# Kernel optimization log

Measured on AMD Instinct MI355X. Metric: run time of the kernel, lower is better.

The kernel has to match this reference:

```python
import jax, jax.numpy as jnp
import numpy as np

ALPHA = 0.2          # LeakyReLU negative slope
ORTHO_LAMBDA = 0.01  # orthogonal regularization weight


def setup_inputs() -> dict:
    key = jax.random.key(0)
    ks = jax.random.split(key, 9)
    N, IN, OUT, NR, H = 50000, 128, 128, 64, 4
    E1, E2 = 200000, 50000
    return {
        "input": jax.random.normal(ks[0], (N, IN), jnp.float32),
        "edge": jax.random.randint(ks[1], (2, E1), 0, N),
        "edge_embed": jax.random.normal(ks[2], (E1, NR), jnp.float32),
        "edge_list_nhop": jax.random.randint(ks[3], (2, E2), 0, N),
        "edge_embed_nhop": jax.random.normal(ks[4], (E2, NR), jnp.float32),
        "proj": jax.random.normal(ks[5], (H, IN, IN), jnp.float32) / np.sqrt(IN).astype(np.float32),
        "W": jax.random.normal(ks[6], (H, OUT, 2 * IN + NR), jnp.float32) * 0.08,
        "a": jax.random.normal(ks[7], (H, 1, OUT), jnp.float32) * 0.1,
        "head_weights": jnp.ones((H,), jnp.float32),
    }


def reference(input, edge, edge_embed, edge_list_nhop, edge_embed_nhop, proj, W, a, head_weights):
    N, IN = input.shape
    H, OUT, _ = W.shape
    e = jnp.concatenate([edge, edge_list_nhop], axis=1)              # [2, E]
    emb = jnp.concatenate([edge_embed, edge_embed_nhop], axis=0)     # [E, NR]
    src, tgt = e[0], e[1]

    # per-head orthogonal projections: head_input[h] = input @ proj[h].T -> [H, N, IN]
    hin = jnp.einsum('ni,hoi->hno', input, proj)

    # edge_m = W @ concat(h_src, h_tgt, rel) without materializing the concat
    W_src, W_tgt, W_rel = W[:, :, :IN], W[:, :, IN:2 * IN], W[:, :, 2 * IN:]
    edge_m = (jnp.einsum('hei,hoi->heo', hin[:, src, :], W_src)
              + jnp.einsum('hei,hoi->heo', hin[:, tgt, :], W_tgt)
              + jnp.einsum('er,hor->heo', emb, W_rel))               # [H, E, OUT]

    scores = jnp.einsum('heo,ho->he', edge_m, a[:, 0, :])            # [H, E]
    powers = -jnp.where(scores > 0, scores, ALPHA * scores)         # -leakyrelu
    edge_e = jnp.exp(powers)                                         # [H, E]

    seg = lambda v: jax.ops.segment_sum(v, src, num_segments=N)
    e_rowsum = jnp.clip(jax.vmap(seg)(edge_e), 1e-12, None)          # [H, N]

    edge_w = edge_e[:, :, None] * edge_m                             # [H, E, OUT]
    head_out = jax.vmap(seg)(edge_w)                                 # [H, N, OUT]

    w = jax.nn.softmax(head_weights)
    out = jnp.einsum('h,hnd->nd', w, head_out)                       # [N, OUT]
    # faithful to torch: divides by the LAST head's e_rowsum (loop leakage)
    out = out / e_rowsum[-1][:, None]

    pp = jnp.einsum('hij,hkj->hik', proj, proj)                      # proj @ proj.T
    eye = jnp.eye(proj.shape[1], dtype=proj.dtype)
    orth_reg = ORTHO_LAMBDA * jnp.sum(jnp.sqrt(jnp.sum((pp - eye) ** 2, axis=(1, 2))))

    return jax.nn.elu(out), orth_reg
```

## Files before the change

### kernel.cpp

```cpp
#include <hip/hip_runtime.h>
#include <math.h>


#define NHEAD 4

typedef unsigned short u16;
typedef __attribute__((ext_vector_type(4))) unsigned short u16x4;
typedef __attribute__((ext_vector_type(8))) unsigned short u16x8;
typedef __attribute__((ext_vector_type(8))) short bf16x8;
typedef __attribute__((ext_vector_type(4))) float f32x4;

__device__ __forceinline__ float bf2f(u16 v) {
    union { unsigned u; float f; } x; x.u = ((unsigned)v) << 16; return x.f;
}
__device__ __forceinline__ u16 f2bf(float f) {
    union { float f; unsigned u; } x; x.f = f;
    const unsigned r = x.u + 0x7FFFu + ((x.u >> 16) & 1u);
    return (u16)(r >> 16);
}

__global__ __launch_bounds__(256) void k1_prep(
    const float* __restrict__ proj, const float* __restrict__ W,
    const float* __restrict__ a, const float* __restrict__ hw,
    u16* __restrict__ M_bf,
    float* __restrict__ asrc, float* __restrict__ atgt, float* __restrict__ arel,
    u16* __restrict__ WcatT_bf, float* __restrict__ wsoft,
    float* __restrict__ orth_part)
{
    __shared__ float projS[128*132];
    __shared__ float WS[32*132];
    __shared__ float tS[128];
    __shared__ float red[256];
    const int h = blockIdx.x;
    const int part = blockIdx.y;
    const int z = blockIdx.z;
    const int tid = threadIdx.x;
    if (part < 2 && z >= 4) return;
    const float* projH = proj + h*(128*128);
    const float* WH = W + h*(128*320);
    const float* aH = a + h*128;

    {
        const float4* p4 = (const float4*)projH;
        for (int idx = tid; idx < 4096; idx += 256)
            *(float4*)&projS[(idx>>5)*132 + (idx&31)*4] = p4[idx];
    }

    if (part < 2) {
        const int koff = part ? 128 : 0;
        for (int idx = tid; idx < 1024; idx += 256) {
            const int ol = idx>>5, jq = idx&31;
            *(float4*)&WS[ol*132 + jq*4] = *(const float4*)&WH[(z*32+ol)*320 + koff + jq*4];
        }
        __syncthreads();
        u16* Mout = M_bf + ((size_t)(part*4 + h))*16384;
        for (int idx = tid; idx < 1024; idx += 256) {
            const int ol = idx>>5, jq = idx&31;
            float4 acc; acc.x=0.f; acc.y=0.f; acc.z=0.f; acc.w=0.f;
            for (int i = 0; i < 128; ++i) {
                const float wv = WS[ol*132 + i];
                const float4 pv = *(const float4*)&projS[i*132 + jq*4];
                acc.x += wv*pv.x; acc.y += wv*pv.y; acc.z += wv*pv.z; acc.w += wv*pv.w;
            }
            u16x4 pk; pk.x=f2bf(acc.x); pk.y=f2bf(acc.y); pk.z=f2bf(acc.z); pk.w=f2bf(acc.w);
            *(u16x4*)&Mout[(z*32+ol)*128 + jq*4] = pk;
        }
        if (z == 0) {
            if (tid < 128) {
                float s = 0.f;
                for (int o = 0; o < 128; ++o) s += aH[o]*WH[o*320 + koff + tid];
                tS[tid] = s;
            }
            __syncthreads();
            if (tid < 128) {
                float s = 0.f;
                for (int i = 0; i < 128; ++i) s += tS[i]*projS[i*132 + tid];
                (part ? atgt : asrc)[h*128 + tid] = s;
            }
        }
    } else {
        __syncthreads();
        float local = 0.f;
        const int base = z*2048;
        for (int idx = base + tid; idx < base + 2048; idx += 256) {
            const int i = idx>>7, k = idx&127;
            if (i > k) continue;
            float s = 0.f;
            for (int q = 0; q < 32; ++q) {
                const float4 pi = *(const float4*)&projS[i*132 + q*4];
                const float4 pk = *(const float4*)&projS[k*132 + q*4];
                s += pi.x*pk.x + pi.y*pk.y + pi.z*pk.z + pi.w*pk.w;
            }
            if (i == k) { s -= 1.f; local += s*s; }
            else local += 2.f*s*s;
        }
        red[tid] = local;
        __syncthreads();
        for (int st = 128; st > 0; st >>= 1) {
            if (tid < st) red[tid] += red[tid+st];
            __syncthreads();
        }
        if (tid == 0) atomicAdd(&orth_part[h], red[0]);
        if (z == 0) {
            if (tid < 64) {
                float s = 0.f;
                for (int o = 0; o < 128; ++o) s += aH[o]*WH[o*320 + 256 + tid];
                arel[h*64 + tid] = s;
            }
            for (int idx = tid; idx < 8192; idx += 256) {
                const int r = idx & 63, o = idx >> 6;
                WcatT_bf[(size_t)o*256 + h*64 + r] = f2bf(WH[o*320 + 256 + r]);
            }
            if (h == 0 && tid == 0) {
                const float m = fmaxf(fmaxf(hw[0],hw[1]), fmaxf(hw[2],hw[3]));
                const float e0=expf(hw[0]-m), e1=expf(hw[1]-m), e2=expf(hw[2]-m), e3=expf(hw[3]-m);
                const float s = e0+e1+e2+e3;
                wsoft[0]=e0/s; wsoft[1]=e1/s; wsoft[2]=e2/s; wsoft[3]=e3/s;
            }
        }
    }
}

__global__ __launch_bounds__(256) void k0_nodes(
    const float* __restrict__ input, const float* __restrict__ asrc, const float* __restrict__ atgt,
    const int* __restrict__ edge, const int* __restrict__ nhop,
    u16* __restrict__ in_bf, float* __restrict__ s_src, float* __restrict__ s_tgt,
    int* __restrict__ deg, int N, int E1, int E2)
{
    __shared__ float aS[512], tS[512];
    const int tid = threadIdx.x;
    for (int idx = tid; idx < 512; idx += 256) { aS[idx] = asrc[idx]; tS[idx] = atgt[idx]; }
    const int t = blockIdx.x*256 + tid;
    if (t < E1 + E2) {
        const int src = (t < E1) ? edge[t] : nhop[t-E1];
        atomicAdd(&deg[src], 1);
    }
    __syncthreads();
    const int n = t;
    if (n >= N) return;
    const float4* inr = (const float4*)(input + (size_t)n*128);
    u16* ob = in_bf + (size_t)n*128;
    float ss[4] = {0.f,0.f,0.f,0.f}, st[4] = {0.f,0.f,0.f,0.f};
    for (int q = 0; q < 32; ++q) {
        const float4 v = inr[q];
        u16x4 pk; pk.x=f2bf(v.x); pk.y=f2bf(v.y); pk.z=f2bf(v.z); pk.w=f2bf(v.w);
        *(u16x4*)(ob + q*4) = pk;
        #pragma unroll
        for (int hh = 0; hh < 4; ++hh) {
            const float4 av = *(const float4*)&aS[hh*128 + q*4];
            const float4 tv = *(const float4*)&tS[hh*128 + q*4];
            ss[hh] += v.x*av.x + v.y*av.y + v.z*av.z + v.w*av.w;
            st[hh] += v.x*tv.x + v.y*tv.y + v.z*tv.z + v.w*tv.w;
        }
    }
    float4 o1; o1.x=ss[0]; o1.y=ss[1]; o1.z=ss[2]; o1.w=ss[3];
    float4 o2; o2.x=st[0]; o2.y=st[1]; o2.z=st[2]; o2.w=st[3];
    *(float4*)(s_src + (size_t)n*4) = o1;
    *(float4*)(s_tgt + (size_t)n*4) = o2;
}

__global__ __launch_bounds__(256) void k2_mfma(
    const u16* __restrict__ in_bf, const u16* __restrict__ M_bf,
    u16* __restrict__ tbl, int N)
{
    __shared__ u16 MS[16384];
    __shared__ u16 DW[4][16*136];
    const int tid = threadIdx.x;
    const int w = tid >> 6, lane = tid & 63;
    const int bid = blockIdx.x;
    const int chunk = gridDim.x >> 3;
    const int swz = (bid & 7)*chunk + (bid >> 3);
    const int n0 = (swz >> 2)*256;
    const int mat = swz & 3;
    const int m = lane & 15, kg = lane >> 4;

    {
        const u16* Mp = M_bf + (size_t)(4 + mat)*16384;
        for (int c = tid; c < 2048; c += 256) {
            const int row = c >> 4, c16 = c & 15;
            const u16x8 v = *(const u16x8*)(Mp + row*128 + c16*8);
            *(u16x8*)((char*)MS + row*256 + ((c16*16) ^ ((row&7)<<4))) = v;
        }
    }
    __syncthreads();

    bf16x8 fa[8][4];
    #pragma unroll
    for (int nt = 0; nt < 8; ++nt) {
        const int row = nt*16 + m;
        #pragma unroll
        for (int ks = 0; ks < 4; ++ks) {
            const int c16 = ks*4 + kg;
            fa[nt][ks] = *(const bf16x8*)((const char*)MS + row*256 + ((c16*16) ^ ((row&7)<<4)));
        }
    }

    for (int sub = 0; sub < 4; ++sub) {
        const int nrow = n0 + w*64 + sub*16 + m;
        const int nclamp = (nrow < N) ? nrow : (N-1);
        bf16x8 fb[4];
        #pragma unroll
        for (int ks = 0; ks < 4; ++ks)
            fb[ks] = *(const bf16x8*)(in_bf + (size_t)nclamp*128 + ks*32 + kg*8);
        f32x4 acc[8];
        #pragma unroll
        for (int nt = 0; nt < 8; ++nt) { acc[nt][0]=0.f; acc[nt][1]=0.f; acc[nt][2]=0.f; acc[nt][3]=0.f; }
        #pragma unroll
        for (int nt = 0; nt < 8; ++nt)
            #pragma unroll
            for (int ks = 0; ks < 4; ++ks)
                acc[nt] = __builtin_amdgcn_mfma_f32_16x16x32_bf16(fa[nt][ks], fb[ks], acc[nt], 0, 0, 0);
        #pragma unroll
        for (int nt = 0; nt < 8; ++nt) {
            unsigned lo, hi;
            asm("v_cvt_pk_bf16_f32 %0, %1, %2" : "=v"(lo) : "v"(acc[nt][0]), "v"(acc[nt][1]));
            asm("v_cvt_pk_bf16_f32 %0, %1, %2" : "=v"(hi) : "v"(acc[nt][2]), "v"(acc[nt][3]));
            uint2 pk; pk.x = lo; pk.y = hi;
            *(uint2*)&DW[w][m*136 + nt*16 + kg*4] = pk;
        }
        const int nb = n0 + w*64 + sub*16;
        #pragma unroll
        for (int k = 0; k < 4; ++k) {
            const int idx = lane + k*64;
            const int row = idx >> 4, seg = idx & 15;
            const int n = nb + row;
            if (n < N) {
                const bf16x8 v = *(const bf16x8*)&DW[w][row*136 + seg*8];
                *(bf16x8*)(tbl + (size_t)n*512 + mat*128 + seg*8) = v;
            }
        }
    }
}

__global__ __launch_bounds__(1024) void k_scanA(const int* __restrict__ deg, int* __restrict__ offsets,
                                                int* __restrict__ bsum, int* __restrict__ boff,
                                                int* __restrict__ sdone, int N, int nb)
{
    __shared__ int wsumS[16];
    __shared__ int ticketS;
    const int tid = threadIdx.x;
    const int lane = tid & 63, wid = tid >> 6;
    const int i0 = blockIdx.x*4096 + tid*4;
    int a0=0,a1=0,a2=0,a3=0;
    if (i0 + 3 < N) { const int4 t = *(const int4*)(deg + i0); a0=t.x; a1=t.y; a2=t.z; a3=t.w; }
    else { if (i0 < N) a0=deg[i0]; if (i0+1 < N) a1=deg[i0+1]; if (i0+2 < N) a2=deg[i0+2]; }
    const int s1=a0+a1, s2=s1+a2, s3=s2+a3;
    int s = s3;
    #pragma unroll
    for (int d = 1; d < 64; d <<= 1) { const int t = __shfl_up(s, d); if (lane >= d) s += t; }
    if (lane == 63) wsumS[wid] = s;
    __syncthreads();
    if (tid < 16) {
        int t = wsumS[tid];
        #pragma unroll
        for (int d = 1; d < 16; d <<= 1) { const int u = __shfl_up(t, d); if (tid >= d) t += u; }
        wsumS[tid] = t;
    }
    __syncthreads();
    const int ex = (wid ? wsumS[wid-1] : 0) + s - s3;
    if (i0 < N)     offsets[i0]   = ex;
    if (i0+1 < N)   offsets[i0+1] = ex + a0;
    if (i0+2 < N)   offsets[i0+2] = ex + s1;
    if (i0+3 < N)   offsets[i0+3] = ex + s2;
    if (tid == 0) {
        bsum[blockIdx.x] = wsumS[15];
        __threadfence();
        ticketS = atomicAdd(sdone, 1);
    }
    __syncthreads();
    if (ticketS == nb - 1 && tid < 64) {
        const int v = (tid < nb) ? atomicAdd(&bsum[tid], 0) : 0;
        int sv = v;
        #pragma unroll
        for (int d = 1; d < 64; d <<= 1) { const int t = __shfl_up(sv, d); if (tid >= d) sv += t; }
        if (tid < nb) boff[tid] = sv - v;
        if (tid == 63) offsets[N] = sv;
    }
}

__global__ __launch_bounds__(256) void k_fill2(
    const int* __restrict__ edge, const int* __restrict__ nhop,
    const float* __restrict__ emb1, const float* __restrict__ emb2,
    const float* __restrict__ s_src, const float* __restrict__ s_tgt,
    const float* __restrict__ arel,
    const int* __restrict__ offsets, const int* __restrict__ boff, int* __restrict__ cursor,
    int* __restrict__ csr_tgt, float* __restrict__ ee_perm, u16* __restrict__ emb_perm,
    int E1, int E2)
{
    const int tid = threadIdx.x;
    const int g = tid >> 4, l = tid & 15;
    const int E = E1 + E2;
    const float4 ar0 = *(const float4*)(arel + 0*64 + l*4);
    const float4 ar1 = *(const float4*)(arel + 1*64 + l*4);
    const float4 ar2 = *(const float4*)(arel + 2*64 + l*4);
    const float4 ar3 = *(const float4*)(arel + 3*64 + l*4);
    const int ebase = blockIdx.x*256;
    #pragma unroll 4
    for (int it = 0; it < 16; ++it) {
        const int e = ebase + it*16 + g;
        if (e >= E) continue;
        const float4 v = (e < E1) ? *(const float4*)(emb1 + (size_t)e*64 + l*4)
                                  : *(const float4*)(emb2 + (size_t)(e-E1)*64 + l*4);
        u16x4 pk; pk.x=f2bf(v.x); pk.y=f2bf(v.y); pk.z=f2bf(v.z); pk.w=f2bf(v.w);
        float p0 = v.x*ar0.x + v.y*ar0.y + v.z*ar0.z + v.w*ar0.w;
        float p1 = v.x*ar1.x + v.y*ar1.y + v.z*ar1.z + v.w*ar1.w;
        float p2 = v.x*ar2.x + v.y*ar2.y + v.z*ar2.z + v.w*ar2.w;
        float p3 = v.x*ar3.x + v.y*ar3.y + v.z*ar3.z + v.w*ar3.w;
        #pragma unroll
        for (int d = 1; d < 16; d <<= 1) {
            p0 += __shfl_xor(p0, d);
            p1 += __shfl_xor(p1, d);
            p2 += __shfl_xor(p2, d);
            p3 += __shfl_xor(p3, d);
        }
        int p = 0;
        if (l == 0) {
            int src, tgt;
            if (e < E1) { src = edge[e]; tgt = edge[E1+e]; }
            else { const int e2 = e-E1; src = nhop[e2]; tgt = nhop[E2+e2]; }
            const float4 s4 = *(const float4*)(s_src + (size_t)src*4);
            const float4 t4 = *(const float4*)(s_tgt + (size_t)tgt*4);
            float4 eo;
            { const float sc = s4.x+t4.x+p0; eo.x = expf(sc>0.f ? -sc : -0.2f*sc); }
            { const float sc = s4.y+t4.y+p1; eo.y = expf(sc>0.f ? -sc : -0.2f*sc); }
            { const float sc = s4.z+t4.z+p2; eo.z = expf(sc>0.f ? -sc : -0.2f*sc); }
            { const float sc = s4.w+t4.w+p3; eo.w = expf(sc>0.f ? -sc : -0.2f*sc); }
            const int pos = atomicAdd(&cursor[src], 1);
            p = offsets[src] + boff[src>>12] + pos;
            csr_tgt[p] = tgt;
            *(float4*)(ee_perm + (size_t)p*4) = eo;
        }
        p = __shfl(p, tid & 48);
        *(u16x4*)(emb_perm + (size_t)p*64 + l*4) = pk;
    }
}

__global__ __launch_bounds__(256) void k4_gather(
    const float* __restrict__ ee_perm, const int* __restrict__ offsets, const int* __restrict__ boff,
    const int* __restrict__ csr_tgt,
    const u16* __restrict__ emb_perm, const u16* __restrict__ tbl,
    const float* __restrict__ wsoft,
    u16* __restrict__ pout_bf, u16* __restrict__ semb_bf, float* __restrict__ rowsum4,
    int N)
{
    __shared__ float eeS[4][64][4];
    __shared__ int   tgS[4][64];
    const int lane = threadIdx.x & 63;
    const int wv = threadIdx.x >> 6;
    const int n = blockIdx.x*4 + wv;
    if (n >= N) return;
    const int hl = lane >> 4;
    const int hoff = hl*128 + (lane & 15)*8;

    union HT { u16x8 v; unsigned u[4]; };

    float acc[8];
    #pragma unroll
    for (int j = 0; j < 8; ++j) acc[j] = 0.f;
    float sm0=0.f, sm1=0.f, sm2=0.f, sm3=0.f;
    float rsl0=0.f, rsl1=0.f, rsl2=0.f, rsl3=0.f;

    const int start = offsets[n] + boff[n>>12];
    const int end = (n+1 == N) ? offsets[N] : (offsets[n+1] + boff[(n+1)>>12]);
    for (int cb = start; cb < end; cb += 64) {
        const int rem = end - cb;
        const int cnt = rem < 64 ? rem : 64;
        int tgtL = 0;
        float4 eeL; eeL.x=0.f; eeL.y=0.f; eeL.z=0.f; eeL.w=0.f;
        if (lane < cnt) {
            tgtL = csr_tgt[cb + lane];
            eeL  = *(const float4*)(ee_perm + (size_t)(cb + lane)*4);
        }
        rsl0 += eeL.x; rsl1 += eeL.y; rsl2 += eeL.z; rsl3 += eeL.w;
        *(float4*)&eeS[wv][lane][0] = eeL;
        tgS[wv][lane] = tgtL;
        const int cp = (cnt + 3) & ~3;

        HT zz; zz.u[0]=0u; zz.u[1]=0u; zz.u[2]=0u; zz.u[3]=0u;
        HT ht0=zz, ht1=zz, ht2=zz, ht3=zz;
        u16 em0=0, em1=0, em2=0, em3=0;
#define K4_FETCH(J, IDX) { const int tg_ = tgS[wv][IDX]; \
            ht##J.v = *(const u16x8*)(tbl + (size_t)tg_*512 + hoff); \
            em##J = emb_perm[(size_t)(cb + (IDX))*64 + lane]; }
        if (0 < cnt) K4_FETCH(0, 0)
        if (1 < cnt) K4_FETCH(1, 1)
        if (2 < cnt) K4_FETCH(2, 2)
        if (3 < cnt) K4_FETCH(3, 3)

#define K4_STAGE(J) { \
            const float4 ee4 = *(const float4*)&eeS[wv][i+J][0]; \
            const float eh = eeS[wv][i+J][hl]; \
            _Pragma("unroll") \
            for (int p = 0; p < 4; ++p) { \
                union{unsigned u; float f;} lo_, hi_; \
                lo_.u = ht##J.u[p] << 16; hi_.u = ht##J.u[p] & 0xffff0000u; \
                acc[2*p]   += eh*lo_.f; \
                acc[2*p+1] += eh*hi_.f; \
            } \
            const float ev = bf2f(em##J); \
            sm0 += ee4.x*ev; sm1 += ee4.y*ev; sm2 += ee4.z*ev; sm3 += ee4.w*ev; \
            { const int ii = i + 4 + J; if (ii < cnt) K4_FETCH(J, ii) } }

        for (int i = 0; i < cp; i += 4) {
            K4_STAGE(0)
            K4_STAGE(1)
            K4_STAGE(2)
            K4_STAGE(3)
        }
#undef K4_STAGE
#undef K4_FETCH
    }

    #pragma unroll
    for (int d = 1; d < 64; d <<= 1) {
        rsl0 += __shfl_xor(rsl0, d);
        rsl1 += __shfl_xor(rsl1, d);
        rsl2 += __shfl_xor(rsl2, d);
        rsl3 += __shfl_xor(rsl3, d);
    }
    if (lane == 0) {
        float4 r4; r4.x=rsl0; r4.y=rsl1; r4.z=rsl2; r4.w=rsl3;
        *(float4*)(rowsum4 + (size_t)n*4) = r4;
    }

    const float4 ws4 = *(const float4*)wsoft;
    const float wh = (hl==0)?ws4.x:(hl==1)?ws4.y:(hl==2)?ws4.z:ws4.w;
    float p[8];
    #pragma unroll
    for (int j = 0; j < 8; ++j) {
        float pv = wh*acc[j];
        pv += __shfl_xor(pv, 16);
        pv += __shfl_xor(pv, 32);
        p[j] = pv;
    }
    if (hl == 0) {
        u16 pk[8];
        #pragma unroll
        for (int j = 0; j < 8; ++j) pk[j] = f2bf(p[j]);
        *(u16x8*)(pout_bf + (size_t)n*128 + (lane & 15)*8) = *(u16x8*)pk;
    }
    u16* so = semb_bf + (size_t)n*256;
    so[lane]       = f2bf(ws4.x*sm0);
    so[64 + lane]  = f2bf(ws4.y*sm1);
    so[128 + lane] = f2bf(ws4.z*sm2);
    so[192 + lane] = f2bf(ws4.w*sm3);
}

__global__ __launch_bounds__(256) void k5_gemm(
    const u16* __restrict__ semb_bf, const u16* __restrict__ wcatT_bf,
    const u16* __restrict__ M_bf, const u16* __restrict__ in_bf,
    const u16* __restrict__ pout_bf,
    const float* __restrict__ rowsum4, const float* __restrict__ wsoft,
    const float* __restrict__ orth_part,
    float* __restrict__ out, int N)
{
    __shared__ u16 MS[16384];
    __shared__ float DS[64*132];
    const int tid = threadIdx.x;
    if (blockIdx.x == 0 && tid == 0)
        out[(size_t)N*128] = 0.01f*(sqrtf(orth_part[0])+sqrtf(orth_part[1])+sqrtf(orth_part[2])+sqrtf(orth_part[3]));
    const int w = tid >> 6, lane = tid & 63;
    const int m = lane & 15, kg = lane >> 4;
    const int n0 = blockIdx.x*64;

    int row = n0 + w*16 + m; if (row >= N) row = N-1;
    const float4 ws4 = *(const float4*)wsoft;
    const float4 rs4 = *(const float4*)(rowsum4 + (size_t)row*4);
    const float rh[4] = {ws4.x*rs4.x, ws4.y*rs4.y, ws4.z*rs4.z, ws4.w*rs4.w};

    bf16x8 fa[8];
    {
        const u16* ap = semb_bf + (size_t)row*256 + kg*8;
        #pragma unroll
        for (int ks = 0; ks < 8; ++ks) fa[ks] = *(const bf16x8*)(ap + ks*32);
    }
    union IU { bf16x8 v; unsigned u[4]; };
    IU fin[4];
    #pragma unroll
    for (int ksub = 0; ksub < 4; ++ksub)
        fin[ksub].v = *(const bf16x8*)(in_bf + (size_t)row*128 + ksub*32 + kg*8);

    f32x4 acc[8];
    #pragma unroll
    for (int nt = 0; nt < 8; ++nt) { acc[nt][0]=0.f; acc[nt][1]=0.f; acc[nt][2]=0.f; acc[nt][3]=0.f; }

    #pragma unroll
    for (int nt = 0; nt < 8; ++nt) {
        const int o = nt*16 + m;
        const u16* bp = wcatT_bf + (size_t)o*256 + kg*8;
        #pragma unroll
        for (int ks = 0; ks < 8; ++ks) {
            const bf16x8 fb = *(const bf16x8*)(bp + ks*32);
            acc[nt] = __builtin_amdgcn_mfma_f32_16x16x32_bf16(fa[ks], fb, acc[nt], 0, 0, 0);
        }
    }

    for (int h = 0; h < 4; ++h) {
        __syncthreads();
        {
            const u16* Mp = M_bf + (size_t)h*16384;
            for (int c = tid; c < 2048; c += 256) {
                const int r = c >> 4, c16 = c & 15;
                const u16x8 v = *(const u16x8*)(Mp + r*128 + c16*8);
                *(u16x8*)((char*)MS + r*256 + ((c16*16) ^ ((r&7)<<4))) = v;
            }
        }
        bf16x8 fsc[4];
        {
            const float r = rh[h];
            #pragma unroll
            for (int ksub = 0; ksub < 4; ++ksub) {
                IU o;
                #pragma unroll
                for (int p = 0; p < 4; ++p) {
                    union{unsigned u; float f;} lo_, hi_;
                    lo_.u = fin[ksub].u[p] << 16; hi_.u = fin[ksub].u[p] & 0xffff0000u;
                    const float a = lo_.f*r, b = hi_.f*r;
                    unsigned pk;
                    asm("v_cvt_pk_bf16_f32 %0, %1, %2" : "=v"(pk) : "v"(a), "v"(b));
                    o.u[p] = pk;
                }
                fsc[ksub] = o.v;
            }
        }
        __syncthreads();
        #pragma unroll
        for (int nt = 0; nt < 8; ++nt) {
            const int o = nt*16 + m;
            #pragma unroll
            for (int ksub = 0; ksub < 4; ++ksub) {
                const int c16 = ksub*4 + kg;
                const bf16x8 fb = *(const bf16x8*)((const char*)MS + o*256 + ((c16*16) ^ ((o&7)<<4)));
                acc[nt] = __builtin_amdgcn_mfma_f32_16x16x32_bf16(fsc[ksub], fb, acc[nt], 0, 0, 0);
            }
        }
    }

    __syncthreads();
    #pragma unroll
    for (int nt = 0; nt < 8; ++nt) {
        const int o = nt*16 + m;
        const int r0 = w*16 + kg*4;
        #pragma unroll
        for (int r = 0; r < 4; ++r)
            DS[(r0+r)*132 + o] = acc[nt][r];
    }
    __syncthreads();
    for (int idx = tid; idx < 2048; idx += 256) {
        const int rrow = idx >> 5, q = idx & 31;
        const int n = n0 + rrow;
        if (n < N) {
            const float4 d = *(const float4*)&DS[rrow*132 + q*4];
            const u16x4 pb = *(const u16x4*)(pout_bf + (size_t)n*128 + q*4);
            const float rinv = 1.0f / fmaxf(rowsum4[(size_t)n*4 + 3], 1e-12f);
            float v0 = (bf2f(pb.x) + d.x)*rinv;
            float v1 = (bf2f(pb.y) + d.y)*rinv;
            float v2 = (bf2f(pb.z) + d.z)*rinv;
            float v3 = (bf2f(pb.w) + d.w)*rinv;
            v0 = (v0 > 0.f) ? v0 : expm1f(v0);
            v1 = (v1 > 0.f) ? v1 : expm1f(v1);
            v2 = (v2 > 0.f) ? v2 : expm1f(v2);
            v3 = (v3 > 0.f) ? v3 : expm1f(v3);
            float4 r4; r4.x=v0; r4.y=v1; r4.z=v2; r4.w=v3;
            *(float4*)(out + (size_t)n*128 + q*4) = r4;
        }
    }
}

extern "C" void kernel_launch(void* const* d_in, const int* in_sizes, int n_in,
                              void* d_out, int out_size, void* d_ws, size_t ws_size,
                              hipStream_t stream)
{
    const float* input = (const float*)d_in[0];
    const int*   edge  = (const int*)d_in[1];
    const float* emb1  = (const float*)d_in[2];
    const int*   nhop  = (const int*)d_in[3];
    const float* emb2  = (const float*)d_in[4];
    const float* proj  = (const float*)d_in[5];
    const float* W     = (const float*)d_in[6];
    const float* a     = (const float*)d_in[7];
    const float* hw    = (const float*)d_in[8];
    float* out = (float*)d_out;

    const int N  = in_sizes[0] / 128;
    const int E1 = in_sizes[1] / 2;
    const int E2 = in_sizes[3] / 2;
    const int E  = E1 + E2;
    (void)n_in; (void)out_size; (void)ws_size;

    char* wsb = (char*)d_ws;
    size_t off = 0;
    auto alloc = [&](size_t bytes) -> char* {
        char* p = wsb + off;
        off += (bytes + 255) & ~(size_t)255;
        return p;
    };
    u16*   in_bf    = (u16*)alloc((size_t)N*128*2);
    u16*   tbl      = (u16*)alloc((size_t)N*512*2);
    u16*   semb_bf  = (u16*)alloc((size_t)N*256*2);
    u16*   pout_bf  = (u16*)alloc((size_t)N*128*2);
    u16*   emb_perm = (u16*)alloc((size_t)E*64*2);
    float* ee_perm  = (float*)alloc((size_t)E*4*4);
    int*   csr_tgt  = (int*)alloc((size_t)E*4);
    u16*   M_bf     = (u16*)alloc((size_t)8*16384*2);
    u16*   WcatT_bf = (u16*)alloc((size_t)128*256*2);
    float* asrc     = (float*)alloc(512*4);
    float* atgt     = (float*)alloc(512*4);
    float* arel     = (float*)alloc(256*4);
    float* s_src    = (float*)alloc((size_t)N*4*4);
    float* s_tgt    = (float*)alloc((size_t)N*4*4);
    float* wsoft    = (float*)alloc(4*4);
    float* rowsum4  = (float*)alloc((size_t)N*4*4);
    int*   offsets  = (int*)alloc((size_t)(N+1)*4);
    int*   bsum     = (int*)alloc(64*4);
    int*   boff     = (int*)alloc(64*4);
    const size_t zoff0 = off;
    float* orth_part= (float*)alloc(4*4);
    int*   deg      = (int*)alloc((size_t)N*4);
    int*   cursor   = (int*)alloc((size_t)N*4);
    int*   sdone    = (int*)alloc(4);
    const size_t zoff1 = off;

    hipMemsetAsync(wsb + zoff0, 0, zoff1 - zoff0, stream);

    const int nbScan = (N + 4095) / 4096;
    const int nx = (N + 255) / 256;
    const int nk0 = ((E > N ? E : N) + 255) / 256;

    k1_prep<<<dim3(NHEAD,3,8), dim3(256), 0, stream>>>(proj, W, a, hw, M_bf,
                                                       asrc, atgt, arel, WcatT_bf, wsoft, orth_part);
    k0_nodes<<<dim3(nk0), dim3(256), 0, stream>>>(input, asrc, atgt, edge, nhop,
                                                  in_bf, s_src, s_tgt, deg, N, E1, E2);
    k2_mfma<<<dim3(nx*4), dim3(256), 0, stream>>>(in_bf, M_bf, tbl, N);
    k_scanA<<<dim3(nbScan), dim3(1024), 0, stream>>>(deg, offsets, bsum, boff, sdone, N, nbScan);
    k_fill2<<<dim3((E+255)/256), dim3(256), 0, stream>>>(edge, nhop, emb1, emb2, s_src, s_tgt,
                                                         arel, offsets, boff, cursor,
                                                         csr_tgt, ee_perm, emb_perm, E1, E2);
    k4_gather<<<dim3((N+3)/4), dim3(256), 0, stream>>>(ee_perm, offsets, boff, csr_tgt, emb_perm,
                                                       tbl, wsoft, pout_bf, semb_bf, rowsum4, N);
    k5_gemm<<<dim3((N+63)/64), dim3(256), 0, stream>>>(semb_bf, WcatT_bf, M_bf, in_bf, pout_bf,
                                                       rowsum4, wsoft, orth_part, out, N);
}
```

Measured before the change: 245.3 us.

## Enlarge k5 GEMM tile to 256 rows and stage WcatT in shared memory

Each k5 block now handles 256 rows instead of 64, with each wave covering 4 sub-tiles of 16 rows. The WcatT weight matrix is staged through LDS in two halves instead of being read per-lane from global memory. Each M_h load into LDS is thereby reused across four times as many rows, which cuts global and L2 weight traffic and the number of LDS fills. The cost is 128 accumulator registers per thread and a grid four times smaller (about 196 blocks), which may leave part of the GPU idle and lower occupancy.

```diff
diff --git a/kernel.cpp b/kernel.cpp
--- a/kernel.cpp
+++ b/kernel.cpp
@@ -455,43 +455,57 @@
     float* __restrict__ out, int N)
 {
     __shared__ u16 MS[16384];
-    __shared__ float DS[64*132];
+    __shared__ float DW[4][16*132];
     const int tid = threadIdx.x;
     if (blockIdx.x == 0 && tid == 0)
         out[(size_t)N*128] = 0.01f*(sqrtf(orth_part[0])+sqrtf(orth_part[1])+sqrtf(orth_part[2])+sqrtf(orth_part[3]));
     const int w = tid >> 6, lane = tid & 63;
     const int m = lane & 15, kg = lane >> 4;
-    const int n0 = blockIdx.x*64;
-
-    int row = n0 + w*16 + m; if (row >= N) row = N-1;
+    const int n0 = blockIdx.x*256;
+
     const float4 ws4 = *(const float4*)wsoft;
-    const float4 rs4 = *(const float4*)(rowsum4 + (size_t)row*4);
-    const float rh[4] = {ws4.x*rs4.x, ws4.y*rs4.y, ws4.z*rs4.z, ws4.w*rs4.w};
-
-    bf16x8 fa[8];
-    {
-        const u16* ap = semb_bf + (size_t)row*256 + kg*8;
-        #pragma unroll
-        for (int ks = 0; ks < 8; ++ks) fa[ks] = *(const bf16x8*)(ap + ks*32);
-    }
-    union IU { bf16x8 v; unsigned u[4]; };
-    IU fin[4];
-    #pragma unroll
-    for (int ksub = 0; ksub < 4; ++ksub)
-        fin[ksub].v = *(const bf16x8*)(in_bf + (size_t)row*128 + ksub*32 + kg*8);
-
-    f32x4 acc[8];
-    #pragma unroll
-    for (int nt = 0; nt < 8; ++nt) { acc[nt][0]=0.f; acc[nt][1]=0.f; acc[nt][2]=0.f; acc[nt][3]=0.f; }
-
-    #pragma unroll
-    for (int nt = 0; nt < 8; ++nt) {
-        const int o = nt*16 + m;
-        const u16* bp = wcatT_bf + (size_t)o*256 + kg*8;
-        #pragma unroll
-        for (int ks = 0; ks < 8; ++ks) {
-            const bf16x8 fb = *(const bf16x8*)(bp + ks*32);
-            acc[nt] = __builtin_amdgcn_mfma_f32_16x16x32_bf16(fa[ks], fb, acc[nt], 0, 0, 0);
+    int rowS[4];
+    float4 rhS[4];
+    #pragma unroll
+    for (int sub = 0; sub < 4; ++sub) {
+        int r = n0 + w*64 + sub*16 + m; if (r >= N) r = N-1;
+        rowS[sub] = r;
+        const float4 rs = *(const float4*)(rowsum4 + (size_t)r*4);
+        rhS[sub].x = ws4.x*rs.x; rhS[sub].y = ws4.y*rs.y;
+        rhS[sub].z = ws4.z*rs.z; rhS[sub].w = ws4.w*rs.w;
+    }
+
+    f32x4 acc[4][8];
+    #pragma unroll
+    for (int sub = 0; sub < 4; ++sub)
+        #pragma unroll
+        for (int nt = 0; nt < 8; ++nt) { acc[sub][nt][0]=0.f; acc[sub][nt][1]=0.f; acc[sub][nt][2]=0.f; acc[sub][nt][3]=0.f; }
+
+    #pragma unroll
+    for (int half = 0; half < 2; ++half) {
+        __syncthreads();
+        for (int c = tid; c < 2048; c += 256) {
+            const int r = c >> 4, c16 = c & 15;
+            const u16x8 v = *(const u16x8*)(wcatT_bf + (size_t)r*256 + half*128 + c16*8);
+            *(u16x8*)((char*)MS + r*256 + ((c16*16) ^ ((r&7)<<4))) = v;
+        }
+        __syncthreads();
+        #pragma unroll
+        for (int sub = 0; sub < 4; ++sub) {
+            bf16x8 fa[4];
+            const u16* ap = semb_bf + (size_t)rowS[sub]*256 + half*128 + kg*8;
+            #pragma unroll
+            for (int ks = 0; ks < 4; ++ks) fa[ks] = *(const bf16x8*)(ap + ks*32);
+            #pragma unroll
+            for (int nt = 0; nt < 8; ++nt) {
+                const int o = nt*16 + m;
+                #pragma unroll
+                for (int ks = 0; ks < 4; ++ks) {
+                    const int c16 = ks*4 + kg;
+                    const bf16x8 fb = *(const bf16x8*)((const char*)MS + o*256 + ((c16*16) ^ ((o&7)<<4)));
+                    acc[sub][nt] = __builtin_amdgcn_mfma_f32_16x16x32_bf16(fa[ks], fb, acc[sub][nt], 0, 0, 0);
+                }
+            }
         }
     }
 
@@ -505,64 +519,70 @@
                 *(u16x8*)((char*)MS + r*256 + ((c16*16) ^ ((r&7)<<4))) = v;
             }
         }
-        bf16x8 fsc[4];
-        {
-            const float r = rh[h];
+        __syncthreads();
+        #pragma unroll
+        for (int sub = 0; sub < 4; ++sub) {
+            const float rsc = (h==0)?rhS[sub].x:(h==1)?rhS[sub].y:(h==2)?rhS[sub].z:rhS[sub].w;
+            union IU { bf16x8 v; unsigned u[4]; };
+            bf16x8 fsc[4];
+            const u16* ip = in_bf + (size_t)rowS[sub]*128 + kg*8;
             #pragma unroll
-            for (int ksub = 0; ksub < 4; ++ksub) {
+            for (int ks = 0; ks < 4; ++ks) {
+                IU t; t.v = *(const bf16x8*)(ip + ks*32);
                 IU o;
                 #pragma unroll
                 for (int p = 0; p < 4; ++p) {
                     union{unsigned u; float f;} lo_, hi_;
-                    lo_.u = fin[ksub].u[p] << 16; hi_.u = fin[ksub].u[p] & 0xffff0000u;
-                    const float a = lo_.f*r, b = hi_.f*r;
+                    lo_.u = t.u[p] << 16; hi_.u = t.u[p] & 0xffff0000u;
+                    const float a = lo_.f*rsc, b = hi_.f*rsc;
                     unsigned pk;
                     asm("v_cvt_pk_bf16_f32 %0, %1, %2" : "=v"(pk) : "v"(a), "v"(b));
                     o.u[p] = pk;
                 }
-                fsc[ksub] = o.v;
-            }
-        }
-        __syncthreads();
+                fsc[ks] = o.v;
+            }
+            #pragma unroll
+            for (int nt = 0; nt < 8; ++nt) {
+                const int o = nt*16 + m;
+                #pragma unroll
+                for (int ks = 0; ks < 4; ++ks) {
+                    const int c16 = ks*4 + kg;
+                    const bf16x8 fb = *(const bf16x8*)((const char*)MS + o*256 + ((c16*16) ^ ((o&7)<<4)));
+                    acc[sub][nt] = __builtin_amdgcn_mfma_f32_16x16x32_bf16(fsc[ks], fb, acc[sub][nt], 0, 0, 0);
+                }
+            }
+        }
+    }
+
+    #pragma unroll
+    for (int sub = 0; sub < 4; ++sub) {
         #pragma unroll
         for (int nt = 0; nt < 8; ++nt) {
-            const int o = nt*16 + m;
             #pragma unroll
-            for (int ksub = 0; ksub < 4; ++ksub) {
-                const int c16 = ksub*4 + kg;
-                const bf16x8 fb = *(const bf16x8*)((const char*)MS + o*256 + ((c16*16) ^ ((o&7)<<4)));
-                acc[nt] = __builtin_amdgcn_mfma_f32_16x16x32_bf16(fsc[ksub], fb, acc[nt], 0, 0, 0);
-            }
-        }
-    }
-
-    __syncthreads();
-    #pragma unroll
-    for (int nt = 0; nt < 8; ++nt) {
-        const int o = nt*16 + m;
-        const int r0 = w*16 + kg*4;
-        #pragma unroll
-        for (int r = 0; r < 4; ++r)
-            DS[(r0+r)*132 + o] = acc[nt][r];
-    }
-    __syncthreads();
-    for (int idx = tid; idx < 2048; idx += 256) {
-        const int rrow = idx >> 5, q = idx & 31;
-        const int n = n0 + rrow;
-        if (n < N) {
-            const float4 d = *(const float4*)&DS[rrow*132 + q*4];
-            const u16x4 pb = *(const u16x4*)(pout_bf + (size_t)n*128 + q*4);
-            const float rinv = 1.0f / fmaxf(rowsum4[(size_t)n*4 + 3], 1e-12f);
-            float v0 = (bf2f(pb.x) + d.x)*rinv;
-            float v1 = (bf2f(pb.y) + d.y)*rinv;
-            float v2 = (bf2f(pb.z) + d.z)*rinv;
-            float v3 = (bf2f(pb.w) + d.w)*rinv;
-            v0 = (v0 > 0.f) ? v0 : expm1f(v0);
-            v1 = (v1 > 0.f) ? v1 : expm1f(v1);
-            v2 = (v2 > 0.f) ? v2 : expm1f(v2);
-            v3 = (v3 > 0.f) ? v3 : expm1f(v3);
-            float4 r4; r4.x=v0; r4.y=v1; r4.z=v2; r4.w=v3;
-            *(float4*)(out + (size_t)n*128 + q*4) = r4;
+            for (int r = 0; r < 4; ++r)
+                DW[w][(kg*4+r)*132 + nt*16 + m] = acc[sub][nt][r];
+        }
+        const int nb = n0 + w*64 + sub*16;
+        #pragma unroll
+        for (int k = 0; k < 8; ++k) {
+            const int idx = lane + k*64;
+            const int row = idx >> 5, q = idx & 31;
+            const int n = nb + row;
+            if (n < N) {
+                const float4 d = *(const float4*)&DW[w][row*132 + q*4];
+                const u16x4 pb = *(const u16x4*)(pout_bf + (size_t)n*128 + q*4);
+                const float rinv = 1.0f / fmaxf(rowsum4[(size_t)n*4 + 3], 1e-12f);
+                float v0 = (bf2f(pb.x) + d.x)*rinv;
+                float v1 = (bf2f(pb.y) + d.y)*rinv;
+                float v2 = (bf2f(pb.z) + d.z)*rinv;
+                float v3 = (bf2f(pb.w) + d.w)*rinv;
+                v0 = (v0 > 0.f) ? v0 : expm1f(v0);
+                v1 = (v1 > 0.f) ? v1 : expm1f(v1);
+                v2 = (v2 > 0.f) ? v2 : expm1f(v2);
+                v3 = (v3 > 0.f) ? v3 : expm1f(v3);
+                float4 r4; r4.x=v0; r4.y=v1; r4.z=v2; r4.w=v3;
+                *(float4*)(out + (size_t)n*128 + q*4) = r4;
+            }
         }
     }
 }
@@ -638,6 +658,6 @@
                                                          csr_tgt, ee_perm, emb_perm, E1, E2);
     k4_gather<<<dim3((N+3)/4), dim3(256), 0, stream>>>(ee_perm, offsets, boff, csr_tgt, emb_perm,
                                                        tbl, wsoft, pout_bf, semb_bf, rowsum4, N);
-    k5_gemm<<<dim3((N+63)/64), dim3(256), 0, stream>>>(semb_bf, WcatT_bf, M_bf, in_bf, pout_bf,
-                                                       rowsum4, wsoft, orth_part, out, N);
-}
+    k5_gemm<<<dim3(nx), dim3(256), 0, stream>>>(semb_bf, WcatT_bf, M_bf, in_bf, pout_bf,
+                                                rowsum4, wsoft, orth_part, out, N);
+}
```

Result: faster. 238.3 us (-2.9%).
